# Kernel optimization log

Hardware: AMD Instinct MI355X
Metric: run time of the kernel (lower is better)

Reference implementation:

```python
import jax, jax.numpy as jnp
import numpy as np


def setup_inputs() -> dict:
    key = jax.random.key(0)
    k1, k2 = jax.random.split(key)
    B, H, S, D = 2, 16, 2048, 64
    scores = jax.random.normal(k1, (B, H, S, S), dtype=jnp.float32)
    v = jax.random.normal(k2, (B, H, S, D), dtype=jnp.float32)
    return {"scores": scores, "v": v}


def reference(scores, v):
    # softmax over last dim of [B,H,S,S], then contract with V [B,H,S,D]
    prob = jax.nn.softmax(scores, axis=-1)
    return jnp.einsum('bhqk,bhkd->bhqd', prob, v)
```

## Files before the change

### kernel.cpp

```cpp
#include <hip/hip_runtime.h>
#include <hip/hip_bf16.h>

#define NBH     32
#define SEQ     2048
#define DIM     64
#define QBLK    64
#define KBLK    64
#define NCHUNK  (SEQ / KBLK)
#define PSTR    72

typedef __attribute__((ext_vector_type(4))) float f32x4;
typedef __attribute__((ext_vector_type(8))) short bf16x8;

__device__ __forceinline__ unsigned short bfbits(float f) {
    return __builtin_bit_cast(unsigned short, __float2bfloat16(f));
}

__global__ __launch_bounds__(256)
void vprep_kernel(const float* __restrict__ v, unsigned short* __restrict__ wsv)
{
    const int blk = blockIdx.x;
    const int bh  = blk >> 5, t = blk & 31;
    const float* vp = v + ((size_t)bh * SEQ + t * KBLK) * DIM;
    unsigned short* op = wsv + (size_t)blk * 4096;

    for (int fl = threadIdx.x; fl < 512; fl += 256) {
        const int ks = fl >> 8, dt = (fl >> 6) & 3, lane = fl & 63;
        const int g = lane >> 4, c = lane & 15;
        const float* sp = vp + (ks * 32 + g * 8) * DIM + dt * 16 + c;
        bf16x8 frag;
#pragma unroll
        for (int j = 0; j < 8; ++j)
            frag[j] = (short)bfbits(sp[j * DIM]);
        *reinterpret_cast<bf16x8*>(op + fl * 8) = frag;
    }
}

__global__ __launch_bounds__(256, 2)
void softmaxv_kernel(const float* __restrict__ scores,
                     const unsigned short* __restrict__ vfrags,
                     float* __restrict__ out)
{
    __shared__ unsigned short p_lds[4][2][16 * PSTR];
    __shared__ float l_lds[QBLK];

    const int tid  = threadIdx.x;
    const int w    = tid >> 6;
    const int lane = tid & 63;
    const int g    = lane >> 4;
    const int c    = lane & 15;

    const int bid = blockIdx.x;
    const int bh  = bid >> 5;
    const int qb  = bid & 31;
    const int q0  = qb * QBLK;

    const float* sp = scores + ((size_t)bh * SEQ + q0 + w * 16 + g) * SEQ + c * 4;
    const unsigned short* vb = vfrags + (size_t)bh * NCHUNK * 4096 + lane * 8;

    unsigned short* pb0 = &p_lds[w][0][0];
    unsigned short* pb1 = &p_lds[w][1][0];

    float lsum[4] = {0.f, 0.f, 0.f, 0.f};
    f32x4 acc[4];
#pragma unroll
    for (int dt = 0; dt < 4; ++dt) acc[dt] = (f32x4)0.0f;

#define SLOADS(dst, t)                                                         \
    {                                                                          \
        _Pragma("unroll")                                                      \
        for (int i = 0; i < 4; ++i)                                            \
            dst[i] = *reinterpret_cast<const f32x4*>(                          \
                sp + (size_t)(i * 4) * SEQ + (t) * KBLK);                      \
    }

#define VLOAD(vf, t)                                                           \
    {                                                                          \
        const unsigned short* vp = vb + (t) * 4096;                            \
        _Pragma("unroll")                                                      \
        for (int ks = 0; ks < 2; ++ks)                                         \
            _Pragma("unroll")                                                  \
            for (int dt = 0; dt < 4; ++dt)                                     \
                vf[ks][dt] = *reinterpret_cast<const bf16x8*>(                 \
                    vp + (ks * 4 + dt) * 512);                                 \
    }

#define PROC(sreg, pbuf)                                                       \
    {                                                                          \
        _Pragma("unroll")                                                      \
        for (int i = 0; i < 4; ++i) {                                          \
            f32x4 s4 = sreg[i];                                                \
            float p0 = __expf(s4[0]);                                          \
            float p1 = __expf(s4[1]);                                          \
            float p2 = __expf(s4[2]);                                          \
            float p3 = __expf(s4[3]);                                          \
            lsum[i] += (p0 + p1) + (p2 + p3);                                  \
            unsigned lo = (unsigned)bfbits(p0) | ((unsigned)bfbits(p1) << 16); \
            unsigned hi = (unsigned)bfbits(p2) | ((unsigned)bfbits(p3) << 16); \
            *reinterpret_cast<uint2*>(&pbuf[(i * 4 + g) * PSTR + c * 4]) =     \
                make_uint2(lo, hi);                                            \
        }                                                                      \
        _Pragma("unroll")                                                      \
        for (int ks = 0; ks < 2; ++ks) {                                       \
            const bf16x8 a = *reinterpret_cast<const bf16x8*>(                 \
                &pbuf[c * PSTR + ks * 32 + g * 8]);                            \
            _Pragma("unroll")                                                  \
            for (int dt = 0; dt < 4; ++dt)                                     \
                acc[dt] = __builtin_amdgcn_mfma_f32_16x16x32_bf16(             \
                    a, vf[ks][dt], acc[dt], 0, 0, 0);                          \
        }                                                                      \
    }

    f32x4 sA[4], sB[4], sC[4], sD[4];
    bf16x8 vf[2][4];
    SLOADS(sA, 0)
    SLOADS(sB, 1)
    for (int t = 0; t < NCHUNK; t += 4) {
        VLOAD(vf, t)
        if (t + 2 < NCHUNK) SLOADS(sC, t + 2)
        PROC(sA, pb0)
        VLOAD(vf, t + 1)
        if (t + 3 < NCHUNK) SLOADS(sD, t + 3)
        PROC(sB, pb1)
        VLOAD(vf, t + 2)
        if (t + 4 < NCHUNK) SLOADS(sA, t + 4)
        PROC(sC, pb0)
        VLOAD(vf, t + 3)
        if (t + 5 < NCHUNK) SLOADS(sB, t + 5)
        PROC(sD, pb1)
    }
#undef SLOADS
#undef VLOAD
#undef PROC

#pragma unroll
    for (int i = 0; i < 4; ++i) {
        float l = lsum[i];
        l += __shfl_xor(l, 1);
        l += __shfl_xor(l, 2);
        l += __shfl_xor(l, 4);
        l += __shfl_xor(l, 8);
        if (c == 0) l_lds[w * 16 + i * 4 + g] = l;
    }

    float* op = out + ((size_t)bh * SEQ + q0 + w * 16) * DIM;
    float rl[4];
#pragma unroll
    for (int r = 0; r < 4; ++r)
        rl[r] = 1.0f / l_lds[w * 16 + g * 4 + r];
#pragma unroll
    for (int dt = 0; dt < 4; ++dt)
#pragma unroll
        for (int r = 0; r < 4; ++r)
            op[(g * 4 + r) * DIM + dt * 16 + c] = acc[dt][r] * rl[r];
}

extern "C" void kernel_launch(void* const* d_in, const int* in_sizes, int n_in,
                              void* d_out, int out_size, void* d_ws, size_t ws_size,
                              hipStream_t stream)
{
    const float* scores = (const float*)d_in[0];
    const float* v      = (const float*)d_in[1];
    float* out          = (float*)d_out;
    unsigned short* wsv = (unsigned short*)d_ws;

    vprep_kernel<<<dim3(NBH * NCHUNK), dim3(256), 0, stream>>>(v, wsv);
    softmaxv_kernel<<<dim3(NBH * (SEQ / QBLK)), dim3(256), 0, stream>>>(scores, wsv, out);
}
```

Before: 141.0 us.

## Double key chunk width, widen row loads, and swizzle block order

```diff
diff --git a/kernel.cpp b/kernel.cpp
--- a/kernel.cpp
+++ b/kernel.cpp
@@ -5,9 +5,9 @@
 #define SEQ     2048
 #define DIM     64
 #define QBLK    64
-#define KBLK    64
+#define KBLK    128
 #define NCHUNK  (SEQ / KBLK)
-#define PSTR    72
+#define PSTR    136
 
 typedef __attribute__((ext_vector_type(4))) float f32x4;
 typedef __attribute__((ext_vector_type(8))) short bf16x8;
@@ -20,14 +20,14 @@
 void vprep_kernel(const float* __restrict__ v, unsigned short* __restrict__ wsv)
 {
     const int blk = blockIdx.x;
-    const int bh  = blk >> 5, t = blk & 31;
-    const float* vp = v + ((size_t)bh * SEQ + t * KBLK) * DIM;
+    const int bh  = blk >> 5, tau = blk & 31;
+    const float* vp = v + ((size_t)bh * SEQ + tau * 64) * DIM;
     unsigned short* op = wsv + (size_t)blk * 4096;
 
     for (int fl = threadIdx.x; fl < 512; fl += 256) {
-        const int ks = fl >> 8, dt = (fl >> 6) & 3, lane = fl & 63;
+        const int ks1 = fl >> 8, dt = (fl >> 6) & 3, lane = fl & 63;
         const int g = lane >> 4, c = lane & 15;
-        const float* sp = vp + (ks * 32 + g * 8) * DIM + dt * 16 + c;
+        const float* sp = vp + (ks1 * 32 + g * 8) * DIM + dt * 16 + c;
         bf16x8 frag;
 #pragma unroll
         for (int j = 0; j < 8; ++j)
@@ -42,26 +42,29 @@
                      float* __restrict__ out)
 {
     __shared__ unsigned short p_lds[4][2][16 * PSTR];
-    __shared__ float l_lds[QBLK];
+    __shared__ float l_lds[4][16];
 
     const int tid  = threadIdx.x;
     const int w    = tid >> 6;
     const int lane = tid & 63;
     const int g    = lane >> 4;
     const int c    = lane & 15;
+    const int h    = lane >> 5;
+    const int c2   = lane & 31;
 
     const int bid = blockIdx.x;
-    const int bh  = bid >> 5;
-    const int qb  = bid & 31;
+    const int nb  = (bid & 7) * (NBH * 32 / 8) + (bid >> 3);
+    const int bh  = nb >> 5;
+    const int qb  = nb & 31;
     const int q0  = qb * QBLK;
 
-    const float* sp = scores + ((size_t)bh * SEQ + q0 + w * 16 + g) * SEQ + c * 4;
-    const unsigned short* vb = vfrags + (size_t)bh * NCHUNK * 4096 + lane * 8;
+    const float* sp = scores + ((size_t)bh * SEQ + q0 + w * 16 + h) * SEQ + c2 * 4;
+    const unsigned short* vb = vfrags + (size_t)bh * 32 * 4096 + lane * 8;
 
     unsigned short* pb0 = &p_lds[w][0][0];
     unsigned short* pb1 = &p_lds[w][1][0];
 
-    float lsum[4] = {0.f, 0.f, 0.f, 0.f};
+    float lsum[8] = {0.f, 0.f, 0.f, 0.f, 0.f, 0.f, 0.f, 0.f};
     f32x4 acc[4];
 #pragma unroll
     for (int dt = 0; dt < 4; ++dt) acc[dt] = (f32x4)0.0f;
@@ -69,39 +72,39 @@
 #define SLOADS(dst, t)                                                         \
     {                                                                          \
         _Pragma("unroll")                                                      \
-        for (int i = 0; i < 4; ++i)                                            \
-            dst[i] = *reinterpret_cast<const f32x4*>(                          \
-                sp + (size_t)(i * 4) * SEQ + (t) * KBLK);                      \
+        for (int j = 0; j < 8; ++j)                                            \
+            dst[j] = *reinterpret_cast<const f32x4*>(                          \
+                sp + (size_t)(2 * j) * SEQ + (t) * KBLK);                      \
     }
 
 #define VLOAD(vf, t)                                                           \
     {                                                                          \
-        const unsigned short* vp = vb + (t) * 4096;                            \
         _Pragma("unroll")                                                      \
-        for (int ks = 0; ks < 2; ++ks)                                         \
+        for (int ks = 0; ks < 4; ++ks)                                         \
             _Pragma("unroll")                                                  \
             for (int dt = 0; dt < 4; ++dt)                                     \
                 vf[ks][dt] = *reinterpret_cast<const bf16x8*>(                 \
-                    vp + (ks * 4 + dt) * 512);                                 \
+                    vb + (size_t)(2 * (t) + (ks >> 1)) * 4096 +                \
+                    ((ks & 1) * 4 + dt) * 512);                                \
     }
 
 #define PROC(sreg, pbuf)                                                       \
     {                                                                          \
         _Pragma("unroll")                                                      \
-        for (int i = 0; i < 4; ++i) {                                          \
-            f32x4 s4 = sreg[i];                                                \
+        for (int j = 0; j < 8; ++j) {                                          \
+            f32x4 s4 = sreg[j];                                                \
             float p0 = __expf(s4[0]);                                          \
             float p1 = __expf(s4[1]);                                          \
             float p2 = __expf(s4[2]);                                          \
             float p3 = __expf(s4[3]);                                          \
-            lsum[i] += (p0 + p1) + (p2 + p3);                                  \
+            lsum[j] += (p0 + p1) + (p2 + p3);                                  \
             unsigned lo = (unsigned)bfbits(p0) | ((unsigned)bfbits(p1) << 16); \
             unsigned hi = (unsigned)bfbits(p2) | ((unsigned)bfbits(p3) << 16); \
-            *reinterpret_cast<uint2*>(&pbuf[(i * 4 + g) * PSTR + c * 4]) =     \
+            *reinterpret_cast<uint2*>(&pbuf[(2 * j + h) * PSTR + c2 * 4]) =    \
                 make_uint2(lo, hi);                                            \
         }                                                                      \
         _Pragma("unroll")                                                      \
-        for (int ks = 0; ks < 2; ++ks) {                                       \
+        for (int ks = 0; ks < 4; ++ks) {                                       \
             const bf16x8 a = *reinterpret_cast<const bf16x8*>(                 \
                 &pbuf[c * PSTR + ks * 32 + g * 8]);                            \
             _Pragma("unroll")                                                  \
@@ -111,43 +114,37 @@
         }                                                                      \
     }
 
-    f32x4 sA[4], sB[4], sC[4], sD[4];
-    bf16x8 vf[2][4];
+    f32x4 sA[8], sB[8];
+    bf16x8 vf[4][4];
     SLOADS(sA, 0)
-    SLOADS(sB, 1)
-    for (int t = 0; t < NCHUNK; t += 4) {
+    for (int t = 0; t < NCHUNK; t += 2) {
         VLOAD(vf, t)
-        if (t + 2 < NCHUNK) SLOADS(sC, t + 2)
+        SLOADS(sB, t + 1)
         PROC(sA, pb0)
         VLOAD(vf, t + 1)
-        if (t + 3 < NCHUNK) SLOADS(sD, t + 3)
+        if (t + 2 < NCHUNK) SLOADS(sA, t + 2)
         PROC(sB, pb1)
-        VLOAD(vf, t + 2)
-        if (t + 4 < NCHUNK) SLOADS(sA, t + 4)
-        PROC(sC, pb0)
-        VLOAD(vf, t + 3)
-        if (t + 5 < NCHUNK) SLOADS(sB, t + 5)
-        PROC(sD, pb1)
     }
 #undef SLOADS
 #undef VLOAD
 #undef PROC
 
 #pragma unroll
-    for (int i = 0; i < 4; ++i) {
-        float l = lsum[i];
+    for (int j = 0; j < 8; ++j) {
+        float l = lsum[j];
         l += __shfl_xor(l, 1);
         l += __shfl_xor(l, 2);
         l += __shfl_xor(l, 4);
         l += __shfl_xor(l, 8);
-        if (c == 0) l_lds[w * 16 + i * 4 + g] = l;
+        l += __shfl_xor(l, 16);
+        if (c2 == j) l_lds[w][2 * j + h] = l;
     }
 
     float* op = out + ((size_t)bh * SEQ + q0 + w * 16) * DIM;
     float rl[4];
 #pragma unroll
     for (int r = 0; r < 4; ++r)
-        rl[r] = 1.0f / l_lds[w * 16 + g * 4 + r];
+        rl[r] = 1.0f / l_lds[w][g * 4 + r];
 #pragma unroll
     for (int dt = 0; dt < 4; ++dt)
 #pragma unroll
@@ -164,6 +161,6 @@
     float* out          = (float*)d_out;
     unsigned short* wsv = (unsigned short*)d_ws;
 
-    vprep_kernel<<<dim3(NBH * NCHUNK), dim3(256), 0, stream>>>(v, wsv);
+    vprep_kernel<<<dim3(NBH * 32), dim3(256), 0, stream>>>(v, wsv);
     softmaxv_kernel<<<dim3(NBH * (SEQ / QBLK)), dim3(256), 0, stream>>>(scores, wsv, out);
 }
```

Result: faster. 137.8 us (-2.3%).
